# Optimization experiments

Hardware: AMD Instinct MI355X
Metric: run time of the kernel (lower is better)

## Reference

```python
import jax, jax.numpy as jnp
import numpy as np

B, C, H, W = 8, 1024, 64, 64

def setup_inputs() -> dict:
    key = jax.random.key(0)
    k1, k2, k3, k4 = jax.random.split(key, 4)
    return {
        "prev_key": jax.random.normal(k1, (B, C, H, W), dtype=jnp.float32),
        "prev_value": jax.random.normal(k2, (B, C, H, W), dtype=jnp.float32),
        "curr_key": jax.random.normal(k3, (B, C, H, W), dtype=jnp.float32),
        "curr_value": jax.random.normal(k4, (B, C, H, W), dtype=jnp.float32),
    }


def _get_affinity(mk, qk):
    # mk, qk: [B, CK, N]  (N = H*W)
    CK = mk.shape[1]
    a_sq = jnp.sum(mk * mk, axis=1)[:, :, None]          # [B, N, 1]
    ab = jnp.einsum('bcn,bcm->bnm', mk, qk)              # [B, N, N]
    affinity = (2.0 * ab - a_sq) / jnp.sqrt(jnp.asarray(CK, mk.dtype))
    # softmax over memory positions (dim 1), numerically stable
    return jax.nn.softmax(affinity, axis=1)              # [B, N, N]


def reference(prev_key, prev_value, curr_key, curr_value):
    b, ck, h, w = prev_key.shape
    n = h * w
    mk = prev_key.reshape(b, ck, n)
    qk = curr_key.reshape(b, ck, n)
    affinity = _get_affinity(mk, qk)                     # [B, N, N]
    cv = prev_value.shape[1]
    mo = prev_value.reshape(b, cv, n)                    # [B, CV, N]
    mem = jnp.einsum('bcn,bnm->bcm', mo, affinity)       # [B, CV, N]
    mem = mem.reshape(b, cv, h, w)
    return jnp.concatenate([mem, curr_value], axis=1)    # [B, 2*CV, H, W]
```

## Files before the change

### kernel.cpp

```cpp
#include <hip/hip_runtime.h>
#include <hip/hip_bf16.h>

#define BATCH 8
#define CH    1024
#define NN    4096

typedef __attribute__((ext_vector_type(8))) short bf16x8;
typedef __attribute__((ext_vector_type(4))) float f32x4;
using bf16 = __hip_bfloat16;

struct bhalf4 { bf16 x, y, z, w; };

__device__ __forceinline__ unsigned short f2bfu(float f) {
  bf16 h = __float2bfloat16(f);
  return *reinterpret_cast<unsigned short*>(&h);
}

template <bool ASQ>
__global__ __launch_bounds__(256) void transpose_cast_v(
    const float* __restrict__ in_all, bf16* __restrict__ out_all,
    float* __restrict__ asq_all) {
  int bz = blockIdx.z;
  const float* in = in_all + (size_t)bz * CH * NN;
  bf16* out = out_all + (size_t)bz * NN * CH;

  __shared__ float tile[64][65];
  __shared__ float sqb[16][64];

  int n0 = blockIdx.x * 64;
  int c0 = blockIdx.y * 64;
  int t = threadIdx.x;
  int nc = t & 15;
  int cr = t >> 4;

  float4 sq4 = make_float4(0.f, 0.f, 0.f, 0.f);
#pragma unroll
  for (int i = 0; i < 4; ++i) {
    int c = cr + i * 16;
    float4 v = *(const float4*)(in + (size_t)(c0 + c) * NN + n0 + nc * 4);
    tile[c][nc * 4 + 0] = v.x;
    tile[c][nc * 4 + 1] = v.y;
    tile[c][nc * 4 + 2] = v.z;
    tile[c][nc * 4 + 3] = v.w;
    if (ASQ) {
      sq4.x += v.x * v.x; sq4.y += v.y * v.y;
      sq4.z += v.z * v.z; sq4.w += v.w * v.w;
    }
  }
  if (ASQ) {
    sqb[cr][nc * 4 + 0] = sq4.x;
    sqb[cr][nc * 4 + 1] = sq4.y;
    sqb[cr][nc * 4 + 2] = sq4.z;
    sqb[cr][nc * 4 + 3] = sq4.w;
  }
  __syncthreads();
  if (ASQ && t < 64) {
    float s = 0.f;
#pragma unroll
    for (int i = 0; i < 16; ++i) s += sqb[i][t];
    atomicAdd(&asq_all[(size_t)bz * NN + n0 + t], s);
  }
  int cchunk = t & 7;
  int nb = t >> 3;
#pragma unroll
  for (int p = 0; p < 2; ++p) {
    int n = nb + p * 32;
    bf16x8 o;
#pragma unroll
    for (int j = 0; j < 8; ++j)
      o[j] = (short)f2bfu(tile[cchunk * 8 + j][n]);
    *(bf16x8*)(out + (size_t)(n0 + n) * CH + c0 + cchunk * 8) = o;
  }
}

__global__ __launch_bounds__(256) void convert_cast(
    const float4* __restrict__ in, bhalf4* __restrict__ out) {
  size_t i = (size_t)blockIdx.x * 256 + threadIdx.x;
  float4 v = in[i];
  bhalf4 o;
  o.x = __float2bfloat16(v.x);
  o.y = __float2bfloat16(v.y);
  o.z = __float2bfloat16(v.z);
  o.w = __float2bfloat16(v.w);
  out[i] = o;
}

#define BARR() __builtin_amdgcn_s_barrier()
#define PRIO(x) __builtin_amdgcn_s_setprio(x)
#define LDS_FENCE() do {                                      \
    asm volatile("s_waitcnt lgkmcnt(0)" ::: "memory");        \
    __builtin_amdgcn_sched_barrier(0);                        \
  } while (0)
#define MEM_FENCE() do {                                      \
    asm volatile("" ::: "memory");                            \
    __builtin_amdgcn_sched_barrier(0);                        \
  } while (0)

template <int K, int MODE, int GY>
__global__ __launch_bounds__(512, 2) void gemm_8p(
    const bf16* __restrict__ Aall, const bf16* __restrict__ Ball,
    bf16* __restrict__ Pall, float* __restrict__ Oall,
    const float* __restrict__ asq_all, float* __restrict__ rsum_all) {
  constexpr int NT = K / 64;
  constexpr int NWG = 16 * GY * BATCH;

  int lid = blockIdx.x;
  int swz = (lid & 7) * (NWG >> 3) + (lid >> 3);
  int bz  = swz / (16 * GY);
  int rem = swz - bz * (16 * GY);
  int by = rem >> 4;
  int bx = rem & 15;

  const bf16* Ab = Aall + (size_t)bz * 4096 * 1024 + (size_t)(by * 256) * K;
  const bf16* Bb = Ball + (size_t)bz * 4096 * (size_t)K + (size_t)(bx * 256) * K;

  __shared__ bf16 As[2][256 * 64];
  __shared__ bf16 Bs[2][256 * 64];

  int tid = threadIdx.x;
  int wv = tid >> 6, lane = tid & 63;
  int fl = lane & 15, quad = lane >> 4;
  int wr = wv >> 2, wc = wv & 3;

  int r0 = tid >> 3;
  int c0 = (tid & 7) ^ (r0 & 7);
  int r1 = (512 + tid) >> 3;
  int c1 = ((512 + tid) & 7) ^ (r1 & 7);
  size_t ga0 = (size_t)r0 * K + c0 * 8;
  size_t ga1 = (size_t)r1 * K + c1 * 8;
  int ls0 = wv * 512;
  int ls1 = 4096 + wv * 512;

#define STAGE(MAT, BUF, T, HF) do { if ((T) < NT) {                            \
    const bf16* g_ = (MAT) + (size_t)(HF) * 128 * K + (size_t)(T) * 64;        \
    bf16* d_ = &BUF[(T) & 1][(HF) * 8192];                                     \
    __builtin_amdgcn_global_load_lds(                                          \
        (const __attribute__((address_space(1))) void*)(g_ + ga0),             \
        (__attribute__((address_space(3))) void*)(d_ + ls0), 16, 0, 0);        \
    __builtin_amdgcn_global_load_lds(                                          \
        (const __attribute__((address_space(1))) void*)(g_ + ga1),             \
        (__attribute__((address_space(3))) void*)(d_ + ls1), 16, 0, 0);        \
  } } while (0)

  int flq = fl & 7;
  int k0 = ((0 | quad) ^ flq) * 8;
  int k1 = ((4 | quad) ^ flq) * 8;
  const int rA = wr * 128 + fl;
  const int rB = wc * 64 + fl;

  f32x4 acc[8][4] = {};
  bf16x8 aL[4][2], aH[4][2], bF[4][2];

  STAGE(Bb, Bs, 0, 0);
  STAGE(Bb, Bs, 0, 1);
  STAGE(Ab, As, 0, 0);
  STAGE(Ab, As, 0, 1);
  STAGE(Bb, Bs, 1, 0);
  STAGE(Bb, Bs, 1, 1);
  asm volatile("s_waitcnt vmcnt(4)" ::: "memory");
  BARR();

  for (int t = 0; t < NT; ++t) {
    const bf16* Ac = As[t & 1];
    const bf16* Bc = Bs[t & 1];

#pragma unroll
    for (int mi = 0; mi < 4; ++mi) {
      const bf16* p = Ac + (rA + mi * 16) * 64;
      aL[mi][0] = *(const bf16x8*)(p + k0);
      aL[mi][1] = *(const bf16x8*)(p + k1);
    }
#pragma unroll
    for (int nj = 0; nj < 2; ++nj) {
      const bf16* p = Bc + (rB + nj * 16) * 64;
      bF[nj][0] = *(const bf16x8*)(p + k0);
      bF[nj][1] = *(const bf16x8*)(p + k1);
    }
    STAGE(Ab, As, t + 1, 0);
    BARR();
    asm volatile("s_waitcnt lgkmcnt(0)" ::: "memory");
    __builtin_amdgcn_sched_barrier(0);
    PRIO(1);
#pragma unroll
    for (int mi = 0; mi < 4; ++mi)
#pragma unroll
      for (int nj = 0; nj < 2; ++nj)
#pragma unroll
        for (int ks = 0; ks < 2; ++ks)
          acc[mi][nj] = __builtin_amdgcn_mfma_f32_16x16x32_bf16(
              aL[mi][ks], bF[nj][ks], acc[mi][nj], 0, 0, 0);
    PRIO(0);
    BARR();

#pragma unroll
    for (int nj = 2; nj < 4; ++nj) {
      const bf16* p = Bc + (rB + nj * 16) * 64;
      bF[nj][0] = *(const bf16x8*)(p + k0);
      bF[nj][1] = *(const bf16x8*)(p + k1);
    }
    STAGE(Ab, As, t + 1, 1);
    BARR();
    asm volatile("s_waitcnt lgkmcnt(0)" ::: "memory");
    __builtin_amdgcn_sched_barrier(0);
    PRIO(1);
#pragma unroll
    for (int mi = 0; mi < 4; ++mi)
#pragma unroll
      for (int nj = 2; nj < 4; ++nj)
#pragma unroll
        for (int ks = 0; ks < 2; ++ks)
          acc[mi][nj] = __builtin_amdgcn_mfma_f32_16x16x32_bf16(
              aL[mi][ks], bF[nj][ks], acc[mi][nj], 0, 0, 0);
    PRIO(0);
    BARR();

#pragma unroll
    for (int mi = 0; mi < 4; ++mi) {
      const bf16* p = Ac + (rA + 64 + mi * 16) * 64;
      aH[mi][0] = *(const bf16x8*)(p + k0);
      aH[mi][1] = *(const bf16x8*)(p + k1);
    }
    STAGE(Bb, Bs, t + 2, 0);
    BARR();
    asm volatile("s_waitcnt lgkmcnt(0)" ::: "memory");
    __builtin_amdgcn_sched_barrier(0);
    PRIO(1);
#pragma unroll
    for (int mi = 0; mi < 4; ++mi)
#pragma unroll
      for (int nj = 2; nj < 4; ++nj)
#pragma unroll
        for (int ks = 0; ks < 2; ++ks)
          acc[mi + 4][nj] = __builtin_amdgcn_mfma_f32_16x16x32_bf16(
              aH[mi][ks], bF[nj][ks], acc[mi + 4][nj], 0, 0, 0);
    PRIO(0);
    BARR();

    STAGE(Bb, Bs, t + 2, 1);
    BARR();
    PRIO(1);
#pragma unroll
    for (int mi = 0; mi < 4; ++mi)
#pragma unroll
      for (int nj = 0; nj < 2; ++nj)
#pragma unroll
        for (int ks = 0; ks < 2; ++ks)
          acc[mi + 4][nj] = __builtin_amdgcn_mfma_f32_16x16x32_bf16(
              aH[mi][ks], bF[nj][ks], acc[mi + 4][nj], 0, 0, 0);
    PRIO(0);
    if (t + 2 < NT) {
      asm volatile("s_waitcnt vmcnt(4)" ::: "memory");
    } else {
      asm volatile("s_waitcnt vmcnt(0)" ::: "memory");
    }
    BARR();
  }
#undef STAGE

  __syncthreads();

  int colbase = bx * 256 + wc * 64;
  int rowg0 = by * 256 + wr * 128;

  if constexpr (MODE == 0) {
    const float* asq = asq_all + (size_t)bz * NN;
    float* rsum = rsum_all + (size_t)bz * NN;
    bf16* P = Pall + (size_t)bz * NN * NN;
    short* scr = (short*)(&As[0][0]) + wv * 1024;

    float aq[4];
#pragma unroll
    for (int nj = 0; nj < 4; ++nj) aq[nj] = asq[colbase + nj * 16 + fl];

    float rs[8][4];
#pragma unroll
    for (int mi = 0; mi < 8; ++mi)
#pragma unroll
      for (int r = 0; r < 4; ++r) rs[mi][r] = 0.f;

#pragma unroll
    for (int mi = 0; mi < 8; ++mi) {
#pragma unroll
      for (int nj = 0; nj < 4; ++nj)
#pragma unroll
        for (int r = 0; r < 4; ++r) {
          int row = (quad << 2) + r;
          float e = __expf((2.f * acc[mi][nj][r] - aq[nj]) * 0.03125f);
          rs[mi][r] += e;
          int chunk = (nj * 2 + (fl >> 3)) ^ (row & 7);
          scr[row * 64 + chunk * 8 + (fl & 7)] = (short)f2bfu(e);
        }
      LDS_FENCE();
#pragma unroll
      for (int p = 0; p < 2; ++p) {
        int row = (p << 3) + (lane >> 3);
        int c = lane & 7;
        int chunk = c ^ (row & 7);
        bf16x8 v = *(const bf16x8*)(scr + row * 64 + chunk * 8);
        *(bf16x8*)(P + (size_t)(rowg0 + mi * 16 + row) * NN + colbase + c * 8) = v;
      }
      MEM_FENCE();
    }
#pragma unroll
    for (int mi = 0; mi < 8; ++mi)
#pragma unroll
      for (int r = 0; r < 4; ++r) {
        float v = rs[mi][r];
        v += __shfl_xor(v, 1);
        v += __shfl_xor(v, 2);
        v += __shfl_xor(v, 4);
        v += __shfl_xor(v, 8);
        if (fl == 0)
          atomicAdd(&rsum[rowg0 + mi * 16 + (quad << 2) + r], v);
      }
  } else {
    float* Co = Oall + (size_t)bz * 2 * CH * NN;
    const float* rsum = rsum_all + (size_t)bz * NN;
    float* scr = (float*)(&As[0][0]) + wv * 1024;

    float inv[4];
#pragma unroll
    for (int nj = 0; nj < 4; ++nj) inv[nj] = 1.f / rsum[colbase + nj * 16 + fl];

#pragma unroll
    for (int mi = 0; mi < 8; ++mi) {
#pragma unroll
      for (int nj = 0; nj < 4; ++nj)
#pragma unroll
        for (int r = 0; r < 4; ++r) {
          int row = (quad << 2) + r;
          int chunk = (nj * 4 + (fl >> 2)) ^ (row & 15);
          scr[row * 64 + chunk * 4 + (fl & 3)] = acc[mi][nj][r] * inv[nj];
        }
      LDS_FENCE();
#pragma unroll
      for (int p = 0; p < 4; ++p) {
        int row = (p << 2) + (lane >> 4);
        int c = lane & 15;
        int chunk = c ^ (row & 15);
        f32x4 v = *(const f32x4*)(scr + row * 64 + chunk * 4);
        *(f32x4*)(Co + (size_t)(rowg0 + mi * 16 + row) * NN + colbase + c * 4) = v;
      }
      MEM_FENCE();
    }
  }
}

__global__ __launch_bounds__(256) void copy_curr(
    const float4* __restrict__ src, float4* __restrict__ dst) {
  size_t idx = (size_t)blockIdx.x * 256 + threadIdx.x;
  size_t b = idx >> 20;
  size_t r = idx & 1048575;
  dst[b * 2097152 + 1048576 + r] = src[idx];
}

extern "C" void kernel_launch(void* const* d_in, const int* in_sizes, int n_in,
                              void* d_out, int out_size, void* d_ws, size_t ws_size,
                              hipStream_t stream) {
  const float* prev_key   = (const float*)d_in[0];
  const float* prev_value = (const float*)d_in[1];
  const float* curr_key   = (const float*)d_in[2];
  const float* curr_value = (const float*)d_in[3];
  float* out = (float*)d_out;

  char* ws = (char*)d_ws;
  bf16* P     = (bf16*)(ws);
  bf16* mk_t  = (bf16*)(ws + 268435456u);
  bf16* qk_t  = (bf16*)(ws + 335544320u);
  bf16* mo_b  = (bf16*)(ws + 402653184u);
  float* a_sq = (float*)(ws + 469762048u);
  float* rsum = a_sq + (size_t)BATCH * NN;

  hipMemsetAsync(a_sq, 0, 2ull * BATCH * NN * sizeof(float), stream);

  transpose_cast_v<true><<<dim3(NN / 64, CH / 64, BATCH), 256, 0, stream>>>(
      prev_key, mk_t, a_sq);
  transpose_cast_v<false><<<dim3(NN / 64, CH / 64, BATCH), 256, 0, stream>>>(
      curr_key, qk_t, nullptr);
  convert_cast<<<(size_t)BATCH * CH * NN / 4 / 256, 256, 0, stream>>>(
      (const float4*)prev_value, (bhalf4*)mo_b);

  gemm_8p<CH, 0, 16><<<dim3(16 * 16 * BATCH), dim3(512), 0, stream>>>(
      qk_t, mk_t, P, nullptr, a_sq, rsum);

  gemm_8p<NN, 1, 4><<<dim3(16 * 4 * BATCH), dim3(512), 0, stream>>>(
      mo_b, P, nullptr, out, nullptr, rsum);

  copy_curr<<<(size_t)BATCH * CH * NN / 4 / 256, 256, 0, stream>>>(
      (const float4*)curr_value, (float4*)out);
}
```

Measured before the change: 1.431 ms.

## Replace 256x256 8-wave GEMM with 128x128 triple-buffered 4-wave GEMM

Replaces the 256x256-tile, 512-thread, double-buffered GEMM with a 128x128-tile, 256-thread kernel that uses a 32-wide K step, triple-buffered LDS and grouped tile swizzling. Smaller tiles and less LDS allow three workgroups per CU and a simpler single-phase main loop, aiming for better occupancy and latency hiding. In exchange, arithmetic intensity per tile drops, so global and L2 traffic rise, and each K step has more barrier overhead relative to its MFMA work.

```diff
diff --git a/kernel.cpp b/kernel.cpp
--- a/kernel.cpp
+++ b/kernel.cpp
@@ -96,87 +96,90 @@
     __builtin_amdgcn_sched_barrier(0);                        \
   } while (0)
 
-template <int K, int MODE, int GY>
-__global__ __launch_bounds__(512, 2) void gemm_8p(
+__device__ __forceinline__ void gload16(const bf16* g, bf16* l) {
+  __builtin_amdgcn_global_load_lds(
+      (const __attribute__((address_space(1))) void*)g,
+      (__attribute__((address_space(3))) void*)l, 16, 0, 0);
+}
+
+template <int K, int MODE, int TM, int TN>
+__global__ __launch_bounds__(256, 3) void gemm_s3(
     const bf16* __restrict__ Aall, const bf16* __restrict__ Ball,
     bf16* __restrict__ Pall, float* __restrict__ Oall,
     const float* __restrict__ asq_all, float* __restrict__ rsum_all) {
-  constexpr int NT = K / 64;
-  constexpr int NWG = 16 * GY * BATCH;
+  constexpr int NT = K / 32;
+  constexpr int TPB = TM * TN;
+  constexpr int NWG = TPB * BATCH;
+  constexpr int GRP = 8;
 
   int lid = blockIdx.x;
   int swz = (lid & 7) * (NWG >> 3) + (lid >> 3);
-  int bz  = swz / (16 * GY);
-  int rem = swz - bz * (16 * GY);
-  int by = rem >> 4;
-  int bx = rem & 15;
-
-  const bf16* Ab = Aall + (size_t)bz * 4096 * 1024 + (size_t)(by * 256) * K;
-  const bf16* Bb = Ball + (size_t)bz * 4096 * (size_t)K + (size_t)(bx * 256) * K;
-
-  __shared__ bf16 As[2][256 * 64];
-  __shared__ bf16 Bs[2][256 * 64];
+  int bz  = swz / TPB;
+  int rem = swz - bz * TPB;
+  int g  = rem / (GRP * TN);
+  int r2 = rem - g * (GRP * TN);
+  int bx = r2 / GRP;
+  int by = g * GRP + (r2 & (GRP - 1));
+
+  const bf16* Ab = Aall + (size_t)bz * TM * 128 * K + (size_t)(by * 128) * K;
+  const bf16* Bb = Ball + (size_t)bz * TN * 128 * K + (size_t)(bx * 128) * K;
+
+  __shared__ bf16 As[3][128 * 32];
+  __shared__ bf16 Bs[3][128 * 32];
+  bf16* const AsB = &As[0][0];
+  bf16* const BsB = &Bs[0][0];
 
   int tid = threadIdx.x;
   int wv = tid >> 6, lane = tid & 63;
   int fl = lane & 15, quad = lane >> 4;
-  int wr = wv >> 2, wc = wv & 3;
-
-  int r0 = tid >> 3;
-  int c0 = (tid & 7) ^ (r0 & 7);
-  int r1 = (512 + tid) >> 3;
-  int c1 = ((512 + tid) & 7) ^ (r1 & 7);
-  size_t ga0 = (size_t)r0 * K + c0 * 8;
-  size_t ga1 = (size_t)r1 * K + c1 * 8;
+  int wr = wv >> 1, wc = wv & 1;
+
+  int r0 = tid >> 2;
+  int c0 = (tid & 3) ^ ((r0 >> 1) & 3);
+  int r1 = (256 + tid) >> 2;
+  int c1 = ((256 + tid) & 3) ^ ((r1 >> 1) & 3);
+  const bf16* gA0 = Ab + (size_t)r0 * K + c0 * 8;
+  const bf16* gA1 = Ab + (size_t)r1 * K + c1 * 8;
+  const bf16* gB0 = Bb + (size_t)r0 * K + c0 * 8;
+  const bf16* gB1 = Bb + (size_t)r1 * K + c1 * 8;
   int ls0 = wv * 512;
-  int ls1 = 4096 + wv * 512;
-
-#define STAGE(MAT, BUF, T, HF) do { if ((T) < NT) {                            \
-    const bf16* g_ = (MAT) + (size_t)(HF) * 128 * K + (size_t)(T) * 64;        \
-    bf16* d_ = &BUF[(T) & 1][(HF) * 8192];                                     \
-    __builtin_amdgcn_global_load_lds(                                          \
-        (const __attribute__((address_space(1))) void*)(g_ + ga0),             \
-        (__attribute__((address_space(3))) void*)(d_ + ls0), 16, 0, 0);        \
-    __builtin_amdgcn_global_load_lds(                                          \
-        (const __attribute__((address_space(1))) void*)(g_ + ga1),             \
-        (__attribute__((address_space(3))) void*)(d_ + ls1), 16, 0, 0);        \
-  } } while (0)
-
-  int flq = fl & 7;
-  int k0 = ((0 | quad) ^ flq) * 8;
-  int k1 = ((4 | quad) ^ flq) * 8;
-  const int rA = wr * 128 + fl;
-  const int rB = wc * 64 + fl;
-
-  f32x4 acc[8][4] = {};
-  bf16x8 aL[4][2], aH[4][2], bF[4][2];
-
-  STAGE(Bb, Bs, 0, 0);
-  STAGE(Bb, Bs, 0, 1);
-  STAGE(Ab, As, 0, 0);
-  STAGE(Ab, As, 0, 1);
-  STAGE(Bb, Bs, 1, 0);
-  STAGE(Bb, Bs, 1, 1);
+  int ls1 = 2048 + wv * 512;
+
+  int kq = (quad ^ ((fl >> 1) & 3)) * 8;
+  int aoff = (wr * 64 + fl) * 32 + kq;
+  int boff = (wc * 64 + fl) * 32 + kq;
+
+  f32x4 acc[4][4] = {};
+
+#define STAGE2() do {                                                         \
+    bf16* da = AsB + sb * 4096;                                               \
+    bf16* db = BsB + sb * 4096;                                               \
+    gload16(gA0, da + ls0); gload16(gA1, da + ls1);                           \
+    gload16(gB0, db + ls0); gload16(gB1, db + ls1);                           \
+    gA0 += 32; gA1 += 32; gB0 += 32; gB1 += 32;                               \
+  } while (0)
+
+  {
+    int sb = 0; STAGE2();
+    sb = 1; STAGE2();
+  }
   asm volatile("s_waitcnt vmcnt(4)" ::: "memory");
   BARR();
 
+  int cb = 0, sb = 2;
   for (int t = 0; t < NT; ++t) {
-    const bf16* Ac = As[t & 1];
-    const bf16* Bc = Bs[t & 1];
-
-#pragma unroll
-    for (int mi = 0; mi < 4; ++mi) {
-      const bf16* p = Ac + (rA + mi * 16) * 64;
-      aL[mi][0] = *(const bf16x8*)(p + k0);
-      aL[mi][1] = *(const bf16x8*)(p + k1);
-    }
-#pragma unroll
-    for (int nj = 0; nj < 2; ++nj) {
-      const bf16* p = Bc + (rB + nj * 16) * 64;
-      bF[nj][0] = *(const bf16x8*)(p + k0);
-      bF[nj][1] = *(const bf16x8*)(p + k1);
-    }
-    STAGE(Ab, As, t + 1, 0);
+    const bf16* Ac = AsB + cb * 4096;
+    const bf16* Bc = BsB + cb * 4096;
+    bf16x8 aF[4], bF[4];
+#pragma unroll
+    for (int mi = 0; mi < 4; ++mi)
+      aF[mi] = *(const bf16x8*)(Ac + aoff + mi * 512);
+#pragma unroll
+    for (int nj = 0; nj < 4; ++nj)
+      bF[nj] = *(const bf16x8*)(Bc + boff + nj * 512);
+
+    if (t + 2 < NT) STAGE2();
+
     BARR();
     asm volatile("s_waitcnt lgkmcnt(0)" ::: "memory");
     __builtin_amdgcn_sched_barrier(0);
@@ -184,69 +187,9 @@
 #pragma unroll
     for (int mi = 0; mi < 4; ++mi)
 #pragma unroll
-      for (int nj = 0; nj < 2; ++nj)
-#pragma unroll
-        for (int ks = 0; ks < 2; ++ks)
-          acc[mi][nj] = __builtin_amdgcn_mfma_f32_16x16x32_bf16(
-              aL[mi][ks], bF[nj][ks], acc[mi][nj], 0, 0, 0);
-    PRIO(0);
-    BARR();
-
-#pragma unroll
-    for (int nj = 2; nj < 4; ++nj) {
-      const bf16* p = Bc + (rB + nj * 16) * 64;
-      bF[nj][0] = *(const bf16x8*)(p + k0);
-      bF[nj][1] = *(const bf16x8*)(p + k1);
-    }
-    STAGE(Ab, As, t + 1, 1);
-    BARR();
-    asm volatile("s_waitcnt lgkmcnt(0)" ::: "memory");
-    __builtin_amdgcn_sched_barrier(0);
-    PRIO(1);
-#pragma unroll
-    for (int mi = 0; mi < 4; ++mi)
-#pragma unroll
-      for (int nj = 2; nj < 4; ++nj)
-#pragma unroll
-        for (int ks = 0; ks < 2; ++ks)
-          acc[mi][nj] = __builtin_amdgcn_mfma_f32_16x16x32_bf16(
-              aL[mi][ks], bF[nj][ks], acc[mi][nj], 0, 0, 0);
-    PRIO(0);
-    BARR();
-
-#pragma unroll
-    for (int mi = 0; mi < 4; ++mi) {
-      const bf16* p = Ac + (rA + 64 + mi * 16) * 64;
-      aH[mi][0] = *(const bf16x8*)(p + k0);
-      aH[mi][1] = *(const bf16x8*)(p + k1);
-    }
-    STAGE(Bb, Bs, t + 2, 0);
-    BARR();
-    asm volatile("s_waitcnt lgkmcnt(0)" ::: "memory");
-    __builtin_amdgcn_sched_barrier(0);
-    PRIO(1);
-#pragma unroll
-    for (int mi = 0; mi < 4; ++mi)
-#pragma unroll
-      for (int nj = 2; nj < 4; ++nj)
-#pragma unroll
-        for (int ks = 0; ks < 2; ++ks)
-          acc[mi + 4][nj] = __builtin_amdgcn_mfma_f32_16x16x32_bf16(
-              aH[mi][ks], bF[nj][ks], acc[mi + 4][nj], 0, 0, 0);
-    PRIO(0);
-    BARR();
-
-    STAGE(Bb, Bs, t + 2, 1);
-    BARR();
-    PRIO(1);
-#pragma unroll
-    for (int mi = 0; mi < 4; ++mi)
-#pragma unroll
-      for (int nj = 0; nj < 2; ++nj)
-#pragma unroll
-        for (int ks = 0; ks < 2; ++ks)
-          acc[mi + 4][nj] = __builtin_amdgcn_mfma_f32_16x16x32_bf16(
-              aH[mi][ks], bF[nj][ks], acc[mi + 4][nj], 0, 0, 0);
+      for (int nj = 0; nj < 4; ++nj)
+        acc[mi][nj] = __builtin_amdgcn_mfma_f32_16x16x32_bf16(
+            aF[mi], bF[nj], acc[mi][nj], 0, 0, 0);
     PRIO(0);
     if (t + 2 < NT) {
       asm volatile("s_waitcnt vmcnt(4)" ::: "memory");
@@ -254,32 +197,35 @@
       asm volatile("s_waitcnt vmcnt(0)" ::: "memory");
     }
     BARR();
-  }
-#undef STAGE
+
+    cb = (cb == 2) ? 0 : cb + 1;
+    sb = (sb == 2) ? 0 : sb + 1;
+  }
+#undef STAGE2
 
   __syncthreads();
 
-  int colbase = bx * 256 + wc * 64;
-  int rowg0 = by * 256 + wr * 128;
+  int colbase = bx * 128 + wc * 64;
+  int rowg0 = by * 128 + wr * 64;
 
   if constexpr (MODE == 0) {
     const float* asq = asq_all + (size_t)bz * NN;
     float* rsum = rsum_all + (size_t)bz * NN;
     bf16* P = Pall + (size_t)bz * NN * NN;
-    short* scr = (short*)(&As[0][0]) + wv * 1024;
+    short* scr = (short*)AsB + wv * 1024;
 
     float aq[4];
 #pragma unroll
     for (int nj = 0; nj < 4; ++nj) aq[nj] = asq[colbase + nj * 16 + fl];
 
-    float rs[8][4];
-#pragma unroll
-    for (int mi = 0; mi < 8; ++mi)
+    float rs[4][4];
+#pragma unroll
+    for (int mi = 0; mi < 4; ++mi)
 #pragma unroll
       for (int r = 0; r < 4; ++r) rs[mi][r] = 0.f;
 
 #pragma unroll
-    for (int mi = 0; mi < 8; ++mi) {
+    for (int mi = 0; mi < 4; ++mi) {
 #pragma unroll
       for (int nj = 0; nj < 4; ++nj)
 #pragma unroll
@@ -302,7 +248,7 @@
       MEM_FENCE();
     }
 #pragma unroll
-    for (int mi = 0; mi < 8; ++mi)
+    for (int mi = 0; mi < 4; ++mi)
 #pragma unroll
       for (int r = 0; r < 4; ++r) {
         float v = rs[mi][r];
@@ -316,14 +262,14 @@
   } else {
     float* Co = Oall + (size_t)bz * 2 * CH * NN;
     const float* rsum = rsum_all + (size_t)bz * NN;
-    float* scr = (float*)(&As[0][0]) + wv * 1024;
+    float* scr = (float*)AsB + wv * 1024;
 
     float inv[4];
 #pragma unroll
     for (int nj = 0; nj < 4; ++nj) inv[nj] = 1.f / rsum[colbase + nj * 16 + fl];
 
 #pragma unroll
-    for (int mi = 0; mi < 8; ++mi) {
+    for (int mi = 0; mi < 4; ++mi) {
 #pragma unroll
       for (int nj = 0; nj < 4; ++nj)
 #pragma unroll
@@ -380,10 +326,10 @@
   convert_cast<<<(size_t)BATCH * CH * NN / 4 / 256, 256, 0, stream>>>(
       (const float4*)prev_value, (bhalf4*)mo_b);
 
-  gemm_8p<CH, 0, 16><<<dim3(16 * 16 * BATCH), dim3(512), 0, stream>>>(
+  gemm_s3<CH, 0, 32, 32><<<dim3(32 * 32 * BATCH), dim3(256), 0, stream>>>(
       qk_t, mk_t, P, nullptr, a_sq, rsum);
 
-  gemm_8p<NN, 1, 4><<<dim3(16 * 4 * BATCH), dim3(512), 0, stream>>>(
+  gemm_s3<NN, 1, 8, 32><<<dim3(8 * 32 * BATCH), dim3(256), 0, stream>>>(
       mo_b, P, nullptr, out, nullptr, rsum);
 
   copy_curr<<<(size_t)BATCH * CH * NN / 4 / 256, 256, 0, stream>>>(
```

New measurement: 1.266 ms. -11.6%, faster.
